# Kernel tuning notes

Measured on AMD Instinct MI355X. Metric: run time of the kernel, lower is better.

Reference implementation:

```python
import jax, jax.numpy as jnp
import numpy as np


def setup_inputs() -> dict:
    key = jax.random.key(0)
    k1, k2, k3, k4, k5 = jax.random.split(key, 5)
    B, Cin, D, H, W = 16, 16, 32, 32, 32
    Cout, Kd = 32, 3
    return {
        "x": jax.random.normal(k1, (B, Cin, D, H, W), dtype=jnp.float32),
        "weight": jax.random.normal(k2, (Cout, Cin, Kd, Kd, Kd), dtype=jnp.float32),
        "conv_bias": jax.random.normal(k3, (Cout,), dtype=jnp.float32),
        "scaling_factor": jax.random.normal(k4, (Cout, 1, 1, 1), dtype=jnp.float32),
        "bias_param": jax.random.normal(k5, (Cout, 1, 1, 1), dtype=jnp.float32),
    }


def reference(x, weight, conv_bias, scaling_factor, bias_param):
    # 3D valid conv, stride 1, NCDHW layout / OIDHW kernel
    y = jax.lax.conv_general_dilated(
        x, weight,
        window_strides=(1, 1, 1),
        padding="VALID",
        dimension_numbers=("NCDHW", "OIDHW", "NCDHW"),
    )
    # per-channel bias, scale, tanh, scale, sigmoid (broadcast over D,H,W)
    y = y + conv_bias[None, :, None, None, None]
    y = jnp.tanh(y * scaling_factor[None]) * bias_param[None]
    return jax.nn.sigmoid(y)
```

## Files before the change

kernel.cpp:

```cpp
#include <hip/hip_runtime.h>

#define NB    16
#define CIN   16
#define COUT  32
#define DIN   32
#define DOUT  30

typedef __attribute__((ext_vector_type(8)))  short        short8;
typedef __attribute__((ext_vector_type(4)))  unsigned int uint4v;
typedef __attribute__((ext_vector_type(16))) float        f32x16;

static __device__ __forceinline__ unsigned short f2bf_rne(float f) {
    unsigned int u = __builtin_bit_cast(unsigned int, f);
    u += 0x7fffu + ((u >> 16) & 1u);
    return (unsigned short)(u >> 16);
}
static __device__ __forceinline__ float bf2f(unsigned short s) {
    unsigned int u = ((unsigned int)s) << 16;
    return __builtin_bit_cast(float, u);
}
static __device__ __forceinline__ unsigned int cvt_pk_bf16(float a, float b) {
    unsigned int r;
    asm("v_cvt_pk_bf16_f32 %0, %1, %2" : "=v"(r) : "v"(a), "v"(b));
    return r;
}

__global__ __launch_bounds__(64) void repack_w(const float* __restrict__ wgt,
                                               short* __restrict__ ws) {
    const int s  = blockIdx.x;
    const int l  = threadIdx.x;
    const int co  = l & 31;
    const int ci0 = (l >> 5) * 8;
    short8 vh, vl;
#pragma unroll
    for (int j = 0; j < 8; ++j) {
        float f = wgt[co * (CIN * 27) + (ci0 + j) * 27 + s];
        unsigned short h = f2bf_rne(f);
        vh[j] = (short)h;
        vl[j] = (short)f2bf_rne(f - bf2f(h));
    }
    ((short8*)ws)[s * 64 + l]            = vh;
    ((short8*)ws)[27 * 64 + s * 64 + l]  = vl;
}

__global__ __launch_bounds__(512) void conv3d_mfma(
    const float* __restrict__ x,
    const short* __restrict__ wsA,
    const float* __restrict__ cbias,
    const float* __restrict__ scal,
    const float* __restrict__ bpar,
    float* __restrict__ out)
{
    __shared__ __align__(16) short sx[2 * 12288];
    __shared__ float sp[96];

    const int htile = blockIdx.x;
    const int dpair = blockIdx.y;
    const int b     = blockIdx.z;

    const int tid  = threadIdx.x;
    const int ww   = tid >> 6;
    const int wd   = ww >> 2;
    const int wy   = ww & 3;
    const int lane = tid & 63;

    if (tid < 32) {
        sp[tid]      = cbias[tid];
        sp[32 + tid] = scal[tid];
        sp[64 + tid] = bpar[tid];
    }

    const int h0 = htile * 4;
    const int d0 = dpair * 2;

    const int xb = b * (CIN * DIN * DIN * DIN);
    for (int c = tid; c < 1536; c += 512) {
        const int w   = c & 31;
        const int hi8 = (c >> 5) & 1;
        const int rr  = c >> 6;
        const int dz  = rr / 6;
        const int row = rr - dz * 6;
        int h_in = h0 + row; if (h_in > 31) h_in = 31;
        const int gbase = xb + (hi8 * 8) * (DIN * DIN * DIN)
                        + (d0 + dz) * (DIN * DIN) + h_in * DIN + w;
        float f[8];
#pragma unroll
        for (int j = 0; j < 8; ++j) f[j] = x[gbase + j * (DIN * DIN * DIN)];
        uint4v vh, vl;
#pragma unroll
        for (int j = 0; j < 8; j += 2) {
            unsigned int hp = cvt_pk_bf16(f[j], f[j + 1]);
            float b0 = __builtin_bit_cast(float, hp << 16);
            float b1 = __builtin_bit_cast(float, hp & 0xffff0000u);
            unsigned int lp = cvt_pk_bf16(f[j] - b0, f[j + 1] - b1);
            vh[j >> 1] = hp;
            vl[j >> 1] = lp;
        }
        const int idx = rr * 64 + hi8 * 32 + w;
        *(uint4v*)(sx + idx * 8)             = vh;
        *(uint4v*)(sx + 12288 + idx * 8)     = vl;
    }
    __syncthreads();

    const int h = h0 + wy;
    if (h >= DOUT) return;
    const int d = d0 + wd;

    const int n  = lane & 31;
    const int hi = lane >> 5;

    int wofs[3];
#pragma unroll
    for (int kw = 0; kw < 3; ++kw) {
        int wc = n + kw; if (wc > 31) wc = 31;
        wofs[kw] = hi * 256 + wc * 8;
    }

    f32x16 acc;
#pragma unroll
    for (int i = 0; i < 16; ++i) acc[i] = 0.0f;

    const short8* wa = (const short8*)wsA;
#pragma unroll
    for (int kd = 0; kd < 3; ++kd) {
#pragma unroll
        for (int kh = 0; kh < 3; ++kh) {
            const int rbase = ((wd + kd) * 6 + wy + kh) * 512;
#pragma unroll
            for (int kw = 0; kw < 3; ++kw) {
                const int s = kd * 9 + kh * 3 + kw;
                short8 ah = wa[s * 64 + lane];
                short8 al = wa[1728 + s * 64 + lane];
                short8 bh = *(const short8*)(sx + rbase + wofs[kw]);
                short8 bl = *(const short8*)(sx + 12288 + rbase + wofs[kw]);
                acc = __builtin_amdgcn_mfma_f32_32x32x16_bf16(ah, bh, acc, 0, 0, 0);
                acc = __builtin_amdgcn_mfma_f32_32x32x16_bf16(ah, bl, acc, 0, 0, 0);
                acc = __builtin_amdgcn_mfma_f32_32x32x16_bf16(al, bh, acc, 0, 0, 0);
            }
        }
    }

    if (n < DOUT) {
        const int obase = b * (COUT * DOUT * DOUT * DOUT)
                        + d * (DOUT * DOUT) + h * DOUT + n;
#pragma unroll
        for (int r = 0; r < 16; ++r) {
            const int co = (r & 3) + 8 * (r >> 2) + 4 * hi;
            float y  = acc[r] + sp[co];
            float t  = y * sp[32 + co];
            float th = 1.0f - 2.0f / (__expf(2.0f * t) + 1.0f);
            float z  = th * sp[64 + co];
            float rr = 1.0f / (1.0f + __expf(-z));
            out[obase + co * (DOUT * DOUT * DOUT)] = rr;
        }
    }
}

extern "C" void kernel_launch(void* const* d_in, const int* in_sizes, int n_in,
                              void* d_out, int out_size, void* d_ws, size_t ws_size,
                              hipStream_t stream) {
    const float* x     = (const float*)d_in[0];
    const float* wgt   = (const float*)d_in[1];
    const float* cbias = (const float*)d_in[2];
    const float* scal  = (const float*)d_in[3];
    const float* bpar  = (const float*)d_in[4];
    float* out = (float*)d_out;
    short* ws  = (short*)d_ws;

    hipLaunchKernelGGL(repack_w, dim3(27), dim3(64), 0, stream, wgt, ws);
    hipLaunchKernelGGL(conv3d_mfma, dim3(8, 15, NB), dim3(512), 0, stream,
                       x, ws, cbias, scal, bpar, out);
}
```

Measured before the change: 147.6 us.

## Pre-split input to bf16 hi/lo in workspace and stream it into LDS

Adds a separate repack_x pass that converts the whole input once into bf16 high/low planes in the workspace. The conv kernel then fills shared memory with direct global-to-LDS loads instead of redoing the redundant per-block fp32 loads and conversions. The MFMA loop is also restructured: it prefetches the next weight fragments and alternates between two accumulators to break the MFMA dependency chain. The cost is an extra pass that writes and re-reads 32 MiB, and the new path runs only if the workspace is large enough, otherwise it falls back to the old kernel.

```diff
diff --git a/kernel.cpp b/kernel.cpp
--- a/kernel.cpp
+++ b/kernel.cpp
@@ -10,6 +10,10 @@
 typedef __attribute__((ext_vector_type(4)))  unsigned int uint4v;
 typedef __attribute__((ext_vector_type(16))) float        f32x16;
 
+#define XWS_OFS_SHORTS   28672
+#define XWS_PART_SHORTS  8388608
+#define WS_NEED          (57344 + 2ull * 16 * 1024 * 1024)
+
 static __device__ __forceinline__ unsigned short f2bf_rne(float f) {
     unsigned int u = __builtin_bit_cast(unsigned int, f);
     u += 0x7fffu + ((u >> 16) & 1u);
@@ -23,6 +27,11 @@
     unsigned int r;
     asm("v_cvt_pk_bf16_f32 %0, %1, %2" : "=v"(r) : "v"(a), "v"(b));
     return r;
+}
+static __device__ __forceinline__ void gload_lds16(const short* g, short* l) {
+    __builtin_amdgcn_global_load_lds(
+        (const __attribute__((address_space(1))) void*)g,
+        (__attribute__((address_space(3))) void*)l, 16, 0, 0);
 }
 
 __global__ __launch_bounds__(64) void repack_w(const float* __restrict__ wgt,
@@ -43,7 +52,136 @@
     ((short8*)ws)[27 * 64 + s * 64 + l]  = vl;
 }
 
-__global__ __launch_bounds__(512) void conv3d_mfma(
+__global__ __launch_bounds__(256) void repack_x(const float* __restrict__ x,
+                                                short* __restrict__ xws) {
+    const int rp  = blockIdx.x * 4 + (threadIdx.x >> 6);
+    const int l   = threadIdx.x & 63;
+    const int hi8 = l >> 5, w = l & 31;
+    const int b   = rp >> 10;
+    const int dh  = rp & 1023;
+    const int gbase = b * (CIN * 32768) + hi8 * 8 * 32768 + dh * 32 + w;
+    float f[8];
+#pragma unroll
+    for (int j = 0; j < 8; ++j) f[j] = x[gbase + j * 32768];
+    uint4v vh, vl;
+#pragma unroll
+    for (int j = 0; j < 8; j += 2) {
+        unsigned int hp = cvt_pk_bf16(f[j], f[j + 1]);
+        float b0 = __builtin_bit_cast(float, hp << 16);
+        float b1 = __builtin_bit_cast(float, hp & 0xffff0000u);
+        unsigned int lp = cvt_pk_bf16(f[j] - b0, f[j + 1] - b1);
+        vh[j >> 1] = hp;
+        vl[j >> 1] = lp;
+    }
+    ((uint4v*)xws)[rp * 64 + l]               = vh;
+    ((uint4v*)xws)[1048576 + rp * 64 + l]     = vl;
+}
+
+__global__ __launch_bounds__(512, 6) void conv3d_mfma_v2(
+    const short* __restrict__ xws,
+    const short* __restrict__ wsA,
+    const float* __restrict__ cbias,
+    const float* __restrict__ scal,
+    const float* __restrict__ bpar,
+    float* __restrict__ out)
+{
+    __shared__ __align__(16) short sx[2 * 12288];
+    __shared__ float sp[96];
+
+    const int htile = blockIdx.x;
+    const int dpair = blockIdx.y;
+    const int b     = blockIdx.z;
+
+    const int tid  = threadIdx.x;
+    const int ww   = tid >> 6;
+    const int wd   = ww >> 2;
+    const int wy   = ww & 3;
+    const int lane = tid & 63;
+
+    if (tid < 32) {
+        sp[tid]      = cbias[tid];
+        sp[32 + tid] = scal[tid];
+        sp[64 + tid] = bpar[tid];
+    }
+
+    const int h0 = htile * 4;
+    const int d0 = dpair * 2;
+
+#pragma unroll
+    for (int t = 0; t < 3; ++t) {
+        const int rpl = ww + t * 8;
+        const int dz  = rpl / 6;
+        const int row = rpl - dz * 6;
+        int h_in = h0 + row; if (h_in > 31) h_in = 31;
+        const int grp = (b * 32 + (d0 + dz)) * 32 + h_in;
+        const short* g0 = xws + (size_t)grp * 512 + lane * 8;
+        const short* g1 = xws + XWS_PART_SHORTS + (size_t)grp * 512 + lane * 8;
+        gload_lds16(g0, sx + rpl * 512);
+        gload_lds16(g1, sx + 12288 + rpl * 512);
+    }
+    __syncthreads();
+
+    const int h = h0 + wy;
+    if (h >= DOUT) return;
+    const int d = d0 + wd;
+
+    const int n  = lane & 31;
+    const int hi = lane >> 5;
+
+    int wofs[3];
+#pragma unroll
+    for (int kw = 0; kw < 3; ++kw) {
+        int wc = n + kw; if (wc > 31) wc = 31;
+        wofs[kw] = hi * 256 + wc * 8;
+    }
+
+    f32x16 acc0, acc1;
+#pragma unroll
+    for (int i = 0; i < 16; ++i) { acc0[i] = 0.0f; acc1[i] = 0.0f; }
+
+    const short8* wa = (const short8*)wsA;
+    short8 ah = wa[lane];
+    short8 al = wa[1728 + lane];
+#pragma unroll
+    for (int s = 0; s < 27; ++s) {
+        const int kd = s / 9, r9 = s - kd * 9, kh = r9 / 3, kw = r9 - kh * 3;
+        const int rbase = ((wd + kd) * 6 + wy + kh) * 512;
+        short8 bh = *(const short8*)(sx + rbase + wofs[kw]);
+        short8 bl = *(const short8*)(sx + 12288 + rbase + wofs[kw]);
+        const int sn = (s < 26) ? s + 1 : 26;
+        short8 anh = wa[sn * 64 + lane];
+        short8 anl = wa[1728 + sn * 64 + lane];
+        if (s & 1) {
+            acc1 = __builtin_amdgcn_mfma_f32_32x32x16_bf16(ah, bh, acc1, 0, 0, 0);
+            acc1 = __builtin_amdgcn_mfma_f32_32x32x16_bf16(ah, bl, acc1, 0, 0, 0);
+            acc1 = __builtin_amdgcn_mfma_f32_32x32x16_bf16(al, bh, acc1, 0, 0, 0);
+        } else {
+            acc0 = __builtin_amdgcn_mfma_f32_32x32x16_bf16(ah, bh, acc0, 0, 0, 0);
+            acc0 = __builtin_amdgcn_mfma_f32_32x32x16_bf16(ah, bl, acc0, 0, 0, 0);
+            acc0 = __builtin_amdgcn_mfma_f32_32x32x16_bf16(al, bh, acc0, 0, 0, 0);
+        }
+        ah = anh; al = anl;
+    }
+#pragma unroll
+    for (int i = 0; i < 16; ++i) acc0[i] += acc1[i];
+
+    if (n < DOUT) {
+        const int obase = b * (COUT * DOUT * DOUT * DOUT)
+                        + d * (DOUT * DOUT) + h * DOUT + n;
+#pragma unroll
+        for (int r = 0; r < 16; ++r) {
+            const int co = (r & 3) + 8 * (r >> 2) + 4 * hi;
+            float y  = acc0[r] + sp[co];
+            float t  = y * sp[32 + co];
+            float th = 1.0f - 2.0f / (__expf(2.0f * t) + 1.0f);
+            float z  = th * sp[64 + co];
+            float rr = 1.0f / (1.0f + __expf(-z));
+            out[obase + co * (DOUT * DOUT * DOUT)] = rr;
+        }
+    }
+}
+
+__global__ __launch_bounds__(512) void conv3d_mfma_v1(
     const float* __restrict__ x,
     const short* __restrict__ wsA,
     const float* __restrict__ cbias,
@@ -97,8 +235,8 @@
             vl[j >> 1] = lp;
         }
         const int idx = rr * 64 + hi8 * 32 + w;
-        *(uint4v*)(sx + idx * 8)             = vh;
-        *(uint4v*)(sx + 12288 + idx * 8)     = vl;
+        *(uint4v*)(sx + idx * 8)         = vh;
+        *(uint4v*)(sx + 12288 + idx * 8) = vl;
     }
     __syncthreads();
 
@@ -168,6 +306,14 @@
     short* ws  = (short*)d_ws;
 
     hipLaunchKernelGGL(repack_w, dim3(27), dim3(64), 0, stream, wgt, ws);
-    hipLaunchKernelGGL(conv3d_mfma, dim3(8, 15, NB), dim3(512), 0, stream,
-                       x, ws, cbias, scal, bpar, out);
-}
+
+    if (ws_size >= WS_NEED) {
+        short* xws = ws + XWS_OFS_SHORTS;
+        hipLaunchKernelGGL(repack_x, dim3(4096), dim3(256), 0, stream, x, xws);
+        hipLaunchKernelGGL(conv3d_mfma_v2, dim3(8, 15, NB), dim3(512), 0, stream,
+                           xws, ws, cbias, scal, bpar, out);
+    } else {
+        hipLaunchKernelGGL(conv3d_mfma_v1, dim3(8, 15, NB), dim3(512), 0, stream,
+                           x, ws, cbias, scal, bpar, out);
+    }
+}
```

Result: slower. 157.9 us (+7.0%).

## Compute two output depth slices per wave, reusing B tiles across kd

Applied to the files above, without the earlier changes.

Each block now covers four output depth slices instead of two, and each wave computes two adjacent depth outputs with two accumulators. One LDS B fragment per input depth slice is shared across the kd taps of both outputs. Weight fragments for the next kh/kw tap are prefetched into registers, and MFMA issue is wrapped in setprio. The grid shrinks in depth, which removes redundant halo loads. The costs are more LDS and registers per block (launch_bounds 512,4) and an idle wave pair in the last depth tile, since 30 is not a multiple of 4.

```diff
diff --git a/kernel.cpp b/kernel.cpp
--- a/kernel.cpp
+++ b/kernel.cpp
@@ -43,7 +43,7 @@
     ((short8*)ws)[27 * 64 + s * 64 + l]  = vl;
 }
 
-__global__ __launch_bounds__(512) void conv3d_mfma(
+__global__ __launch_bounds__(512, 4) void conv3d_mfma_v10(
     const float* __restrict__ x,
     const short* __restrict__ wsA,
     const float* __restrict__ cbias,
@@ -51,11 +51,11 @@
     const float* __restrict__ bpar,
     float* __restrict__ out)
 {
-    __shared__ __align__(16) short sx[2 * 12288];
+    __shared__ __align__(16) short sx[2 * 18432];
     __shared__ float sp[96];
 
     const int htile = blockIdx.x;
-    const int dpair = blockIdx.y;
+    const int dquad = blockIdx.y;
     const int b     = blockIdx.z;
 
     const int tid  = threadIdx.x;
@@ -71,18 +71,19 @@
     }
 
     const int h0 = htile * 4;
-    const int d0 = dpair * 2;
+    const int d0 = dquad * 4;
 
     const int xb = b * (CIN * DIN * DIN * DIN);
-    for (int c = tid; c < 1536; c += 512) {
+    for (int c = tid; c < 2304; c += 512) {
         const int w   = c & 31;
         const int hi8 = (c >> 5) & 1;
         const int rr  = c >> 6;
         const int dz  = rr / 6;
         const int row = rr - dz * 6;
+        int d_in = d0 + dz; if (d_in > 31) d_in = 31;
         int h_in = h0 + row; if (h_in > 31) h_in = 31;
         const int gbase = xb + (hi8 * 8) * (DIN * DIN * DIN)
-                        + (d0 + dz) * (DIN * DIN) + h_in * DIN + w;
+                        + d_in * (DIN * DIN) + h_in * DIN + w;
         float f[8];
 #pragma unroll
         for (int j = 0; j < 8; ++j) f[j] = x[gbase + j * (DIN * DIN * DIN)];
@@ -97,61 +98,98 @@
             vl[j >> 1] = lp;
         }
         const int idx = rr * 64 + hi8 * 32 + w;
-        *(uint4v*)(sx + idx * 8)             = vh;
-        *(uint4v*)(sx + 12288 + idx * 8)     = vl;
+        *(uint4v*)(sx + idx * 8)         = vh;
+        *(uint4v*)(sx + 18432 + idx * 8) = vl;
     }
     __syncthreads();
 
-    const int h = h0 + wy;
-    if (h >= DOUT) return;
-    const int d = d0 + wd;
+    const int h   = h0 + wy;
+    const int dw0 = d0 + 2 * wd;
+    if (h >= DOUT || dw0 >= DOUT) return;
 
     const int n  = lane & 31;
     const int hi = lane >> 5;
 
-    int wofs[3];
+    const short* pb[3];
 #pragma unroll
     for (int kw = 0; kw < 3; ++kw) {
         int wc = n + kw; if (wc > 31) wc = 31;
-        wofs[kw] = hi * 256 + wc * 8;
-    }
-
-    f32x16 acc;
-#pragma unroll
-    for (int i = 0; i < 16; ++i) acc[i] = 0.0f;
+        pb[kw] = sx + wd * 6144 + wy * 512 + hi * 256 + wc * 8;
+    }
+
+    f32x16 acc0, acc1;
+#pragma unroll
+    for (int i = 0; i < 16; ++i) { acc0[i] = 0.0f; acc1[i] = 0.0f; }
 
     const short8* wa = (const short8*)wsA;
-#pragma unroll
-    for (int kd = 0; kd < 3; ++kd) {
-#pragma unroll
-        for (int kh = 0; kh < 3; ++kh) {
-            const int rbase = ((wd + kd) * 6 + wy + kh) * 512;
-#pragma unroll
-            for (int kw = 0; kw < 3; ++kw) {
-                const int s = kd * 9 + kh * 3 + kw;
-                short8 ah = wa[s * 64 + lane];
-                short8 al = wa[1728 + s * 64 + lane];
-                short8 bh = *(const short8*)(sx + rbase + wofs[kw]);
-                short8 bl = *(const short8*)(sx + 12288 + rbase + wofs[kw]);
-                acc = __builtin_amdgcn_mfma_f32_32x32x16_bf16(ah, bh, acc, 0, 0, 0);
-                acc = __builtin_amdgcn_mfma_f32_32x32x16_bf16(ah, bl, acc, 0, 0, 0);
-                acc = __builtin_amdgcn_mfma_f32_32x32x16_bf16(al, bh, acc, 0, 0, 0);
-            }
+
+    short8 Ah0 = wa[0 * 64 + lane],  Ah1 = wa[9 * 64 + lane],  Ah2 = wa[18 * 64 + lane];
+    short8 Al0 = wa[1728 + 0 * 64 + lane], Al1 = wa[1728 + 9 * 64 + lane],
+           Al2 = wa[1728 + 18 * 64 + lane];
+
+#pragma unroll
+    for (int e = 0; e < 9; ++e) {
+        const int kh = e / 3, kw = e - kh * 3;
+        const int en = (e < 8) ? e + 1 : 8;
+        short8 Anh0 = wa[(0 * 9 + en) * 64 + lane];
+        short8 Anh1 = wa[(1 * 9 + en) * 64 + lane];
+        short8 Anh2 = wa[(2 * 9 + en) * 64 + lane];
+        short8 Anl0 = wa[1728 + (0 * 9 + en) * 64 + lane];
+        short8 Anl1 = wa[1728 + (1 * 9 + en) * 64 + lane];
+        short8 Anl2 = wa[1728 + (2 * 9 + en) * 64 + lane];
+
+        const short* base = pb[kw] + kh * 512;
+        short8 bh = *(const short8*)(base);
+        short8 bl = *(const short8*)(base + 18432);
+#pragma unroll
+        for (int dz = 0; dz < 4; ++dz) {
+            const short8 cbh = bh, cbl = bl;
+            if (dz < 3) {
+                bh = *(const short8*)(base + (dz + 1) * 3072);
+                bl = *(const short8*)(base + 18432 + (dz + 1) * 3072);
+            }
+            __builtin_amdgcn_s_setprio(1);
+            if (dz < 3) {
+                const short8 ah = (dz == 0) ? Ah0 : (dz == 1) ? Ah1 : Ah2;
+                const short8 al = (dz == 0) ? Al0 : (dz == 1) ? Al1 : Al2;
+                acc0 = __builtin_amdgcn_mfma_f32_32x32x16_bf16(ah, cbh, acc0, 0, 0, 0);
+                acc0 = __builtin_amdgcn_mfma_f32_32x32x16_bf16(ah, cbl, acc0, 0, 0, 0);
+                acc0 = __builtin_amdgcn_mfma_f32_32x32x16_bf16(al, cbh, acc0, 0, 0, 0);
+            }
+            if (dz > 0) {
+                const short8 ah = (dz == 1) ? Ah0 : (dz == 2) ? Ah1 : Ah2;
+                const short8 al = (dz == 1) ? Al0 : (dz == 2) ? Al1 : Al2;
+                acc1 = __builtin_amdgcn_mfma_f32_32x32x16_bf16(ah, cbh, acc1, 0, 0, 0);
+                acc1 = __builtin_amdgcn_mfma_f32_32x32x16_bf16(ah, cbl, acc1, 0, 0, 0);
+                acc1 = __builtin_amdgcn_mfma_f32_32x32x16_bf16(al, cbh, acc1, 0, 0, 0);
+            }
+            __builtin_amdgcn_s_setprio(0);
         }
+        Ah0 = Anh0; Ah1 = Anh1; Ah2 = Anh2;
+        Al0 = Anl0; Al1 = Anl1; Al2 = Anl2;
     }
 
     if (n < DOUT) {
         const int obase = b * (COUT * DOUT * DOUT * DOUT)
-                        + d * (DOUT * DOUT) + h * DOUT + n;
+                        + dw0 * (DOUT * DOUT) + h * DOUT + n;
 #pragma unroll
         for (int r = 0; r < 16; ++r) {
             const int co = (r & 3) + 8 * (r >> 2) + 4 * hi;
-            float y  = acc[r] + sp[co];
-            float t  = y * sp[32 + co];
-            float th = 1.0f - 2.0f / (__expf(2.0f * t) + 1.0f);
-            float z  = th * sp[64 + co];
-            float rr = 1.0f / (1.0f + __expf(-z));
-            out[obase + co * (DOUT * DOUT * DOUT)] = rr;
+            const float cb = sp[co], sc = sp[32 + co], bp = sp[64 + co];
+            {
+                float y  = acc0[r] + cb;
+                float t  = y * sc;
+                float th = 1.0f - 2.0f / (__expf(2.0f * t) + 1.0f);
+                float z  = th * bp;
+                out[obase + co * (DOUT * DOUT * DOUT)] = 1.0f / (1.0f + __expf(-z));
+            }
+            {
+                float y  = acc1[r] + cb;
+                float t  = y * sc;
+                float th = 1.0f - 2.0f / (__expf(2.0f * t) + 1.0f);
+                float z  = th * bp;
+                out[obase + (DOUT * DOUT) + co * (DOUT * DOUT * DOUT)] = 1.0f / (1.0f + __expf(-z));
+            }
         }
     }
 }
@@ -168,6 +206,6 @@
     short* ws  = (short*)d_ws;
 
     hipLaunchKernelGGL(repack_w, dim3(27), dim3(64), 0, stream, wgt, ws);
-    hipLaunchKernelGGL(conv3d_mfma, dim3(8, 15, NB), dim3(512), 0, stream,
+    hipLaunchKernelGGL(conv3d_mfma_v10, dim3(8, 8, NB), dim3(512), 0, stream,
                        x, ws, cbias, scal, bpar, out);
 }
```

Result: faster. 134.5 us (-8.9%).
